# Optimization experiments

Hardware: AMD Instinct MI355X
Metric: run time of the kernel (lower is better)

## Reference

```python
import jax, jax.numpy as jnp
import numpy as np

P = 3  # patch_size; propagate_size = 3; stride = 1


def _extract_kernels(background):
    # background: [bz, nc, w, h, d] -> per-position 3x3x3 patches [bz, L, nc, 3,3,3], L = w*h*d
    bz, nc, w, h, d = background.shape
    pad = jnp.pad(background, ((0, 0), (0, 0), (1, 1), (1, 1), (1, 1)))
    shifts = [pad[:, :, i:i + w, j:j + h, k:k + d]
              for i in range(P) for j in range(P) for k in range(P)]  # 27 fixed shifts
    patches = jnp.stack(shifts, axis=-1)                      # [bz, nc, w, h, d, 27]
    patches = patches.reshape(bz, nc, w * h * d, P, P, P)     # matches torch unfold->view
    return patches.transpose(0, 2, 1, 3, 4, 5)                # [bz, L, nc, 3, 3, 3]


def _box_sum(x):
    # depthwise conv with ones[3,3,3], padding 1 (the propagation conv), done separably
    for ax in (2, 3, 4):
        n = x.shape[ax]
        cfg = [(1, 1) if a == ax else (0, 0) for a in range(x.ndim)]
        p = jnp.pad(x, cfg)
        x = (jax.lax.slice_in_dim(p, 0, n, axis=ax)
             + jax.lax.slice_in_dim(p, 1, n + 1, axis=ax)
             + jax.lax.slice_in_dim(p, 2, n + 2, axis=ax))
    return x


def _per_sample(fm, kernels, mask_i):
    # fm: [nc, w, h, d]; kernels: [L, nc, 3,3,3]; mask_i: [1, w, h, d]
    k = kernels + 1e-7
    k = k / jnp.sqrt(jnp.sum(k * k, axis=(1, 2, 3, 4), keepdims=True))
    x = fm[None]  # [1, nc, w, h, d]
    # patch-correlation: conv3d with per-sample dynamic kernels, padding=1 -> [1, L, w, h, d]
    conv_result = jax.lax.conv_general_dilated(x, k, (1, 1, 1), [(1, 1)] * 3)
    conv_result = _box_sum(conv_result)                 # propagation conv (ones kernel)
    attn = jax.nn.softmax(conv_result, axis=1)          # softmax over the L patch channels
    # conv_transpose3d(stride=1, padding=1) == conv3d with spatially flipped, IO-swapped kernel
    kt = jnp.flip(k, axis=(2, 3, 4)).transpose(1, 0, 2, 3, 4)  # [nc, L, 3, 3, 3]
    recovered = jax.lax.conv_general_dilated(attn, kt, (1, 1, 1), [(1, 1)] * 3)[0]  # [nc,w,h,d]
    recovered = recovered * mask_i / float(P ** 3)
    return recovered + fm * (1.0 - mask_i)


def setup_inputs() -> dict:
    key = jax.random.key(0)
    k1, k2 = jax.random.split(key)
    foreground = jax.random.normal(k1, (4, 64, 16, 16, 16), dtype=jnp.float32)
    mask = jnp.round(jax.random.uniform(k2, (4, 1, 16, 16, 16), dtype=jnp.float32))
    return {"foreground": foreground, "mask": mask}


def reference(foreground, mask):
    background = foreground * (1.0 - mask)   # background='same' path
    kernels = _extract_kernels(background)   # [bz, L, nc, 3, 3, 3]
    return jax.vmap(_per_sample)(foreground, kernels, mask)
```

## Files before the change

### kernel.cpp

```cpp
#include <hip/hip_runtime.h>
#include <hip/hip_bf16.h>
#include <math.h>

#define L 4096
#define NC 64
#define BZ 4
#define PS 17
#define PXD 272

typedef __attribute__((ext_vector_type(8))) short bf16x8;
typedef __attribute__((ext_vector_type(4))) float f32x4;

__device__ inline unsigned short f2bf(float f) {
    unsigned int u = __float_as_uint(f);
    return (unsigned short)((u + 0x7fffu + ((u >> 16) & 1u)) >> 16);
}
__device__ inline float bf2f(unsigned int u) { return __uint_as_float(u << 16); }
__device__ inline void unpack8(uint4 v, float* f) {
    f[0] = bf2f(v.x & 0xffffu); f[1] = bf2f(v.x >> 16);
    f[2] = bf2f(v.y & 0xffffu); f[3] = bf2f(v.y >> 16);
    f[4] = bf2f(v.z & 0xffffu); f[5] = bf2f(v.z >> 16);
    f[6] = bf2f(v.w & 0xffffu); f[7] = bf2f(v.w >> 16);
}
__device__ inline uint4 pack8(const float* f) {
    uint4 v;
    v.x = (unsigned)f2bf(f[0]) | ((unsigned)f2bf(f[1]) << 16);
    v.y = (unsigned)f2bf(f[2]) | ((unsigned)f2bf(f[3]) << 16);
    v.z = (unsigned)f2bf(f[4]) | ((unsigned)f2bf(f[5]) << 16);
    v.w = (unsigned)f2bf(f[6]) | ((unsigned)f2bf(f[7]) << 16);
    return v;
}

__device__ void box3_pad(float* A, float* B, int tid, float out[16]) {
    int x = tid >> 4, y = tid & 15;
    int base = x * PXD + y * PS;
    float t[16];
    {
        float line[16];
        #pragma unroll
        for (int z = 0; z < 16; z++) line[z] = A[base + z];
        #pragma unroll
        for (int z = 0; z < 16; z++) {
            float s = line[z];
            if (z > 0)  s += line[z - 1];
            if (z < 15) s += line[z + 1];
            t[z] = s;
        }
    }
    #pragma unroll
    for (int z = 0; z < 16; z++) B[base + z] = t[z];
    __syncthreads();
    #pragma unroll
    for (int z = 0; z < 16; z++) {
        float s = B[base + z];
        if (y > 0)  s += B[base - PS + z];
        if (y < 15) s += B[base + PS + z];
        t[z] = s;
    }
    __syncthreads();
    #pragma unroll
    for (int z = 0; z < 16; z++) A[base + z] = t[z];
    __syncthreads();
    #pragma unroll
    for (int z = 0; z < 16; z++) {
        float s = A[base + z];
        if (x > 0)  s += A[base - PXD + z];
        if (x < 15) s += A[base + PXD + z];
        out[z] = s;
    }
    __syncthreads();
}
__device__ inline void fill_pad(float* A, const float* __restrict__ g, int tid) {
    for (int i = tid; i < 4096; i += 256)
        A[(i >> 8) * PXD + ((i >> 4) & 15) * PS + (i & 15)] = g[i];
    __syncthreads();
}

__global__ void k_prep(const float* __restrict__ fm, const float* __restrict__ mask,
                       unsigned short* __restrict__ bgT, unsigned short* __restrict__ fmT,
                       unsigned short* __restrict__ bgh,
                       float* __restrict__ sfm, float* __restrict__ sbg,
                       float* __restrict__ qbg) {
    int b = blockIdx.y;
    int p = blockIdx.x * 256 + threadIdx.x;
    float m = mask[b * L + p];
    float w = 1.f - m;
    float s_f = 0.f, s_b = 0.f, q_b = 0.f;
    const float* fmb = fm + (size_t)b * NC * L + p;
    unsigned short* bghb = bgh + (size_t)b * NC * L + p;
    unsigned short tA[NC], tB[NC];
    #pragma unroll
    for (int c = 0; c < NC; c++) {
        float f = fmb[(size_t)c * L];
        float g = f * w;
        s_f += f; s_b += g; q_b += g * g;
        unsigned short gb = f2bf(g);
        tA[c] = gb;
        tB[c] = f2bf(f);
        bghb[(size_t)c * L] = gb;
    }
    unsigned short* bgTb = bgT + (size_t)b * L * NC + (size_t)p * NC;
    unsigned short* fmTb = fmT + (size_t)b * L * NC + (size_t)p * NC;
    #pragma unroll
    for (int i = 0; i < 8; i++) {
        ((uint4*)bgTb)[i] = ((const uint4*)tA)[i];
        ((uint4*)fmTb)[i] = ((const uint4*)tB)[i];
    }
    sfm[b * L + p] = s_f;
    sbg[b * L + p] = s_b;
    qbg[b * L + p] = q_b;
}

__global__ void k_stats(const float* __restrict__ sfm, const float* __restrict__ sbg,
                        const float* __restrict__ qbg,
                        float* __restrict__ invn, float* __restrict__ s2fm) {
    __shared__ float A[16 * PXD];
    __shared__ float Bf[16 * PXD];
    int b = blockIdx.x;
    int tid = threadIdx.x;
    int x = tid >> 4, y = tid & 15;
    float Q[16], Sb[16], r[16];

    fill_pad(A, qbg + b * L, tid);
    box3_pad(A, Bf, tid, Q);
    fill_pad(A, sbg + b * L, tid);
    box3_pad(A, Bf, tid, Sb);
    for (int z = 0; z < 16; z++) {
        float denom = Q[z] + 2e-7f * Sb[z] + 1.728e-11f;
        invn[b * L + x * 256 + y * 16 + z] = rsqrtf(denom);
    }
    fill_pad(A, sfm + b * L, tid);
    box3_pad(A, Bf, tid, r);
    int base = x * PXD + y * PS;
    #pragma unroll
    for (int z = 0; z < 16; z++) A[base + z] = r[z];
    __syncthreads();
    box3_pad(A, Bf, tid, r);
    for (int z = 0; z < 16; z++) s2fm[b * L + x * 256 + y * 16 + z] = r[z];
}

__global__ __launch_bounds__(256) void k_gram(const unsigned short* __restrict__ bgT,
                                              const unsigned short* __restrict__ fmT,
                                              unsigned short* __restrict__ slab,
                                              size_t slotU, int b0) {
    int zi = blockIdx.z, b = b0 + zi;
    unsigned short* Czz = slab + (size_t)zi * slotU;
    const unsigned short* bgTb = bgT + (size_t)b * L * NC;
    const unsigned short* fmTb = fmT + (size_t)b * L * NC;
    __shared__ float Gs[64][65];
    __shared__ float D1[64][65];
    int tid = threadIdx.x;
    int l0 = blockIdx.y * 64, p0 = blockIdx.x * 64;
    int w = tid >> 6, lane = tid & 63;
    int rr = lane & 15, kg = lane >> 4;

    bf16x8 a0 = *(const bf16x8*)&bgTb[(size_t)(l0 + w * 16 + rr) * NC + kg * 8];
    bf16x8 a1 = *(const bf16x8*)&bgTb[(size_t)(l0 + w * 16 + rr) * NC + 32 + kg * 8];
    f32x4 acc[4];
    #pragma unroll
    for (int pt = 0; pt < 4; pt++) {
        bf16x8 bb0 = *(const bf16x8*)&fmTb[(size_t)(p0 + pt * 16 + rr) * NC + kg * 8];
        bf16x8 bb1 = *(const bf16x8*)&fmTb[(size_t)(p0 + pt * 16 + rr) * NC + 32 + kg * 8];
        f32x4 z; z[0] = 0.f; z[1] = 0.f; z[2] = 0.f; z[3] = 0.f;
        z = __builtin_amdgcn_mfma_f32_16x16x32_bf16(a0, bb0, z, 0, 0, 0);
        z = __builtin_amdgcn_mfma_f32_16x16x32_bf16(a1, bb1, z, 0, 0, 0);
        acc[pt] = z;
    }
    #pragma unroll
    for (int pt = 0; pt < 4; pt++)
        #pragma unroll
        for (int r = 0; r < 4; r++)
            Gs[w * 16 + kg * 4 + r][pt * 16 + rr] = acc[pt][r];
    __syncthreads();
    for (int i = tid; i < 4096; i += 256) {
        int il = i >> 6, jp = i & 63;
        int lz = il & 15, pz = jp & 15;
        float v = Gs[il][jp];
        if (lz > 0 && pz > 0)   v += Gs[il - 1][jp - 1];
        if (lz < 15 && pz < 15) v += Gs[il + 1][jp + 1];
        D1[il][jp] = v;
    }
    __syncthreads();
    int row = tid >> 2, cg = (tid & 3) * 16;
    float o[16];
    #pragma unroll
    for (int k = 0; k < 16; k++) {
        int jp = cg + k;
        float v = D1[row][jp];
        if (k > 0)  v += D1[row][jp - 1];
        if (k < 15) v += D1[row][jp + 1];
        o[k] = v;
    }
    uint4* dst = (uint4*)&Czz[(size_t)(l0 + row) * L + p0 + cg];
    dst[0] = pack8(o);
    dst[1] = pack8(o + 8);
}

__global__ __launch_bounds__(256) void k_rowE(unsigned short* __restrict__ slab,
                                              size_t slotU,
                                              const float* __restrict__ s2fm,
                                              const float* __restrict__ invn, int b0) {
    __shared__ float A[16 * PXD];
    int zi = blockIdx.z, b = b0 + zi;
    const unsigned short* Czz = slab + (size_t)zi * slotU;
    unsigned short* E = slab + (size_t)zi * slotU + (size_t)L * L;
    int bx = blockIdx.x;
    int l = (bx & 7) * 512 + (bx >> 3);
    int lx = l >> 8, ly = (l >> 4) & 15;
    int tid = threadIdx.x;
    int px = tid >> 4, py = tid & 15;
    float c[16];
    #pragma unroll
    for (int z = 0; z < 16; z++) c[z] = 0.f;

    #pragma unroll
    for (int dx = -1; dx <= 1; dx++) {
        if (lx + dx < 0 || lx + dx > 15 || px + dx < 0 || px + dx > 15) continue;
        #pragma unroll
        for (int dy = -1; dy <= 1; dy++) {
            if (ly + dy < 0 || ly + dy > 15 || py + dy < 0 || py + dy > 15) continue;
            const unsigned short* src = Czz + (size_t)(l + dy * 16 + dx * 256) * L
                                        + (px + dx) * 256 + (py + dy) * 16;
            float f[16];
            unpack8(((const uint4*)src)[0], f);
            unpack8(((const uint4*)src)[1], f + 8);
            #pragma unroll
            for (int z = 0; z < 16; z++) c[z] += f[z];
        }
    }
    int base = px * PXD + py * PS;
    #pragma unroll
    for (int z = 0; z < 16; z++) A[base + z] = c[z];
    __syncthreads();
    float t[16];
    #pragma unroll
    for (int z = 0; z < 16; z++) {
        float s = A[base + z];
        if (py > 0)  s += A[base - PS + z];
        if (py < 15) s += A[base + PS + z];
        t[z] = s;
    }
    __syncthreads();
    #pragma unroll
    for (int z = 0; z < 16; z++) A[base + z] = t[z];
    __syncthreads();
    float inl = invn[(size_t)b * L + l];
    const float* s2 = s2fm + (size_t)b * L + px * 256 + py * 16;
    float o[16];
    #pragma unroll
    for (int z = 0; z < 16; z++) {
        float s = A[base + z];
        if (px > 0)  s += A[base - PXD + z];
        if (px < 15) s += A[base + PXD + z];
        o[z] = __expf((s + 1e-7f * s2[z]) * inl);
    }
    uint4* dst = (uint4*)&E[(size_t)l * L + px * 256 + py * 16];
    dst[0] = pack8(o);
    dst[1] = pack8(o + 8);
}

__global__ void k_colstat_part(unsigned short* __restrict__ slab, size_t slotU,
                               const float* __restrict__ invn, int b0) {
    int zi = blockIdx.z, b = b0 + zi;
    const unsigned short* E = slab + (size_t)zi * slotU + (size_t)L * L;
    float* ps = (float*)(slab + (size_t)zi * slotU);
    float* psi = ps + 64 * (size_t)L;
    int p8 = (blockIdx.x * 256 + threadIdx.x) * 8;
    int lc = blockIdx.y;
    const float* inv = invn + (size_t)b * L + lc * 64;
    float S[8], SI[8];
    #pragma unroll
    for (int j = 0; j < 8; j++) { S[j] = 0.f; SI[j] = 0.f; }
    const unsigned short* eb = E + (size_t)lc * 64 * L + p8;
    for (int i = 0; i < 64; i++) {
        uint4 v = *(const uint4*)(eb + (size_t)i * L);
        float f[8]; unpack8(v, f);
        float iv = inv[i];
        #pragma unroll
        for (int j = 0; j < 8; j++) { S[j] += f[j]; SI[j] += f[j] * iv; }
    }
    float4* d0 = (float4*)(ps + (size_t)lc * L + p8);
    float4* d1 = (float4*)(psi + (size_t)lc * L + p8);
    d0[0] = make_float4(S[0], S[1], S[2], S[3]);
    d0[1] = make_float4(S[4], S[5], S[6], S[7]);
    d1[0] = make_float4(SI[0], SI[1], SI[2], SI[3]);
    d1[1] = make_float4(SI[4], SI[5], SI[6], SI[7]);
}

__global__ void k_colstat_merge(unsigned short* __restrict__ slab, size_t slotU,
                                float* __restrict__ csi, float* __restrict__ Tarr, int b0) {
    int zi = blockIdx.z, b = b0 + zi;
    const float* ps = (const float*)(slab + (size_t)zi * slotU);
    const float* psi = ps + 64 * (size_t)L;
    int p = blockIdx.x * 256 + threadIdx.x;
    float s = 0.f, si = 0.f;
    for (int i = 0; i < 64; i++) { s += ps[(size_t)i * L + p]; si += psi[(size_t)i * L + p]; }
    float inv = 1.f / s;
    csi[(size_t)b * L + p] = inv;
    Tarr[(size_t)b * L + p] = si * inv;
}

__global__ void k_tbox(const float* __restrict__ Tarr, float* __restrict__ Tbox, int b0) {
    __shared__ float A[16 * PXD];
    __shared__ float Bf[16 * PXD];
    int b = b0 + blockIdx.z;
    int tid = threadIdx.x;
    fill_pad(A, Tarr + (size_t)b * L, tid);
    float res[16];
    box3_pad(A, Bf, tid, res);
    int x = tid >> 4, y = tid & 15;
    for (int z = 0; z < 16; z++) Tbox[(size_t)b * L + x * 256 + y * 16 + z] = res[z];
}

__global__ void k_sm_diagz(unsigned short* __restrict__ slab, size_t slotU,
                           const float* __restrict__ csi, const float* __restrict__ invn,
                           int b0) {
    int zi = blockIdx.z, b = b0 + zi;
    const unsigned short* E = slab + (size_t)zi * slotU + (size_t)L * L;
    unsigned short* azz = slab + (size_t)zi * slotU;
    int line = blockIdx.x * 256 + threadIdx.x;
    int l = line >> 8;
    int p0 = (line & 255) * 16;
    int lz = l & 15;
    bool hm = lz > 0, hp = lz < 15;

    float fc[16], fmv[16], fpv[16];
    const uint4* ec = (const uint4*)(E + (size_t)l * L + p0);
    unpack8(ec[0], fc); unpack8(ec[1], fc + 8);
    if (hm) {
        const uint4* em = (const uint4*)(E + (size_t)(l - 1) * L + p0);
        unpack8(em[0], fmv); unpack8(em[1], fmv + 8);
    }
    if (hp) {
        const uint4* ep = (const uint4*)(E + (size_t)(l + 1) * L + p0);
        unpack8(ep[0], fpv); unpack8(ep[1], fpv + 8);
    }
    float cs[16];
    const float4* cp = (const float4*)(csi + (size_t)b * L + p0);
    #pragma unroll
    for (int q = 0; q < 4; q++) {
        float4 v = cp[q];
        cs[q * 4] = v.x; cs[q * 4 + 1] = v.y; cs[q * 4 + 2] = v.z; cs[q * 4 + 3] = v.w;
    }
    float inl = invn[(size_t)b * L + l];
    float inlm = hm ? invn[(size_t)b * L + l - 1] : 0.f;
    float inlp = hp ? invn[(size_t)b * L + l + 1] : 0.f;
    float o[16];
    #pragma unroll
    for (int z = 0; z < 16; z++) {
        float v = fc[z] * cs[z] * inl;
        if (hm && z > 0)  v += fmv[z - 1] * cs[z - 1] * inlm;
        if (hp && z < 15) v += fpv[z + 1] * cs[z + 1] * inlp;
        o[z] = v;
    }
    uint4* dst = (uint4*)&azz[(size_t)l * L + p0];
    dst[0] = pack8(o);
    dst[1] = pack8(o + 8);
}

__global__ __launch_bounds__(256) void k_diag2t(unsigned short* __restrict__ slab,
                                                size_t slotU) {
    __shared__ float T[64][65];
    int zi = blockIdx.z;
    const unsigned short* azz = slab + (size_t)zi * slotU;
    unsigned short* Ht = slab + (size_t)zi * slotU + (size_t)L * L;
    int tid = threadIdx.x;
    int bi = blockIdx.y, bj = blockIdx.x;
    int m0 = bi * 64, p0 = bj * 64;
    int mx = bi >> 2, px = bj >> 2;
    int myb = 4 * (bi & 3), pyb = 4 * (bj & 3);
    int im = tid >> 3;
    int jp8 = (tid & 7) * 8;
    int pcol = pyb + (jp8 >> 4);

    float acc[2][8];
    #pragma unroll
    for (int g = 0; g < 2; g++)
        #pragma unroll
        for (int j = 0; j < 8; j++) acc[g][j] = 0.f;

    #pragma unroll
    for (int dx = -1; dx <= 1; dx++) {
        if (mx + dx < 0 || mx + dx > 15 || px + dx < 0 || px + dx > 15) continue;
        #pragma unroll
        for (int dy = -1; dy <= 1; dy++) {
            if (pcol + dy < 0 || pcol + dy > 15) continue;
            int D = dy * 16 + dx * 256;
            #pragma unroll
            for (int g = 0; g < 2; g++) {
                int m = im + 32 * g;
                int my = myb + (m >> 4);
                if (my + dy < 0 || my + dy > 15) continue;
                uint4 v = *(const uint4*)(azz + (size_t)(m0 + m + D) * L + p0 + jp8 + D);
                float f[8]; unpack8(v, f);
                #pragma unroll
                for (int j = 0; j < 8; j++) acc[g][j] += f[j];
            }
        }
    }
    #pragma unroll
    for (int g = 0; g < 2; g++)
        #pragma unroll
        for (int j = 0; j < 8; j++) T[im + 32 * g][jp8 + j] = acc[g][j];
    __syncthreads();
    int pr = tid >> 2, ms = (tid & 3) * 16;
    float o[16];
    #pragma unroll
    for (int i = 0; i < 16; i++) o[i] = T[ms + i][pr];
    uint4* dst = (uint4*)&Ht[(size_t)(p0 + pr) * L + m0 + ms];
    dst[0] = pack8(o);
    dst[1] = pack8(o + 8);
}

__global__ __launch_bounds__(256) void k_mm(unsigned short* __restrict__ slab, size_t slotU,
                                            const unsigned short* __restrict__ bgh, int b0) {
    int zi = blockIdx.z, b = b0 + zi;
    const unsigned short* Ht = slab + (size_t)zi * slotU + (size_t)L * L;
    float* part = (float*)(slab + (size_t)zi * slotU);
    const unsigned short* bghb = bgh + (size_t)b * NC * L;
    int tid = threadIdx.x;
    int w = tid >> 6, lane = tid & 63;
    int rr = lane & 15, kg = lane >> 4;
    int p0 = blockIdx.x * 64;
    int k0 = blockIdx.y * 512;

    f32x4 acc[4];
    #pragma unroll
    for (int pt = 0; pt < 4; pt++) { acc[pt][0] = 0.f; acc[pt][1] = 0.f; acc[pt][2] = 0.f; acc[pt][3] = 0.f; }

    for (int kk = 0; kk < 16; kk++) {
        int kb = k0 + kk * 32 + kg * 8;
        bf16x8 a = *(const bf16x8*)&bghb[(size_t)(w * 16 + rr) * L + kb];
        #pragma unroll
        for (int pt = 0; pt < 4; pt++) {
            bf16x8 bb = *(const bf16x8*)&Ht[(size_t)(p0 + pt * 16 + rr) * L + kb];
            acc[pt] = __builtin_amdgcn_mfma_f32_16x16x32_bf16(a, bb, acc[pt], 0, 0, 0);
        }
    }
    float* pp = part + (size_t)blockIdx.y * NC * L;
    #pragma unroll
    for (int pt = 0; pt < 4; pt++)
        #pragma unroll
        for (int r = 0; r < 4; r++)
            pp[(size_t)(w * 16 + kg * 4 + r) * L + p0 + pt * 16 + rr] = acc[pt][r];
}

__global__ void k_epilogue(unsigned short* __restrict__ slab, size_t slotU,
                           const float* __restrict__ Tbox, const float* __restrict__ mask,
                           const float* __restrict__ fm, float* __restrict__ out, int b0) {
    int zi = blockIdx.z, b = b0 + zi;
    const float* part = (const float*)(slab + (size_t)zi * slotU);
    int idx4 = (blockIdx.x * 256 + threadIdx.x) * 4;
    int p = idx4 & 4095;
    float4 s = make_float4(0.f, 0.f, 0.f, 0.f);
    #pragma unroll
    for (int i = 0; i < 8; i++) {
        float4 v = *(const float4*)(part + (size_t)i * NC * L + idx4);
        s.x += v.x; s.y += v.y; s.z += v.z; s.w += v.w;
    }
    float4 tb = *(const float4*)(Tbox + (size_t)b * L + p);
    float4 mk = *(const float4*)(mask + (size_t)b * L + p);
    float4 fv = *(const float4*)(fm + (size_t)b * NC * L + idx4);
    float4 o;
    o.x = (s.x + 1e-7f * tb.x) * mk.x * (1.f / 27.f) + fv.x * (1.f - mk.x);
    o.y = (s.y + 1e-7f * tb.y) * mk.y * (1.f / 27.f) + fv.y * (1.f - mk.y);
    o.z = (s.z + 1e-7f * tb.z) * mk.z * (1.f / 27.f) + fv.z * (1.f - mk.z);
    o.w = (s.w + 1e-7f * tb.w) * mk.w * (1.f / 27.f) + fv.w * (1.f - mk.w);
    *(float4*)(out + (size_t)b * NC * L + idx4) = o;
}

extern "C" void kernel_launch(void* const* d_in, const int* in_sizes, int n_in,
                              void* d_out, int out_size, void* d_ws, size_t ws_size,
                              hipStream_t stream) {
    const float* fm = (const float*)d_in[0];
    const float* mask = (const float*)d_in[1];
    float* out = (float*)d_out;

    unsigned short* bgT = (unsigned short*)d_ws;
    unsigned short* fmT = bgT + (size_t)BZ * L * NC;
    unsigned short* bgh = fmT + (size_t)BZ * L * NC;
    float* sfm  = (float*)(bgh + (size_t)BZ * L * NC);
    float* sbg  = sfm + (size_t)BZ * L;
    float* qbg  = sbg + (size_t)BZ * L;
    float* invn = qbg + (size_t)BZ * L;
    float* s2fm = invn + (size_t)BZ * L;
    float* csi  = s2fm + (size_t)BZ * L;
    float* Tarr = csi + (size_t)BZ * L;
    float* Tbox = Tarr + (size_t)BZ * L;
    unsigned short* slab = (unsigned short*)(Tbox + (size_t)BZ * L);

    const size_t slotU = 2 * (size_t)L * L;
    size_t fixedBytes = (char*)slab - (char*)d_ws;
    size_t avail = ws_size > fixedBytes ? ws_size - fixedBytes : 0;
    int ns = (int)(avail / (slotU * sizeof(unsigned short)));
    if (ns >= 4) ns = 4; else if (ns >= 2) ns = 2; else ns = 1;

    k_prep<<<dim3(16, BZ), 256, 0, stream>>>(fm, mask, bgT, fmT, bgh, sfm, sbg, qbg);
    k_stats<<<BZ, 256, 0, stream>>>(sfm, sbg, qbg, invn, s2fm);

    for (int b0 = 0; b0 < BZ; b0 += ns) {
        int nb = (BZ - b0) < ns ? (BZ - b0) : ns;
        k_gram<<<dim3(64, 64, nb), 256, 0, stream>>>(bgT, fmT, slab, slotU, b0);
        k_rowE<<<dim3(4096, 1, nb), 256, 0, stream>>>(slab, slotU, s2fm, invn, b0);
        k_colstat_part<<<dim3(2, 64, nb), 256, 0, stream>>>(slab, slotU, invn, b0);
        k_colstat_merge<<<dim3(16, 1, nb), 256, 0, stream>>>(slab, slotU, csi, Tarr, b0);
        k_tbox<<<dim3(1, 1, nb), 256, 0, stream>>>(Tarr, Tbox, b0);
        k_sm_diagz<<<dim3(4096, 1, nb), 256, 0, stream>>>(slab, slotU, csi, invn, b0);
        k_diag2t<<<dim3(64, 64, nb), 256, 0, stream>>>(slab, slotU);
        k_mm<<<dim3(64, 8, nb), 256, 0, stream>>>(slab, slotU, bgh, b0);
        k_epilogue<<<dim3(256, 1, nb), 256, 0, stream>>>(slab, slotU, Tbox, mask, fm, out, b0);
    }
}
```

Baseline: 653.4 us.

## Batch stencil loads into predicated registers and drop shared-memory passes

Several kernels change at once. In k_rowE and k_diag2t, the nine stencil loads are now issued up front with clamped addresses and 0/1 weights, so they can all be in flight together instead of each sitting behind a branch. k_rowE also does its y-direction box sum with warp shuffles rather than a shared-memory round trip, and k_gram fuses two stencil passes into one so the D1 buffer and a barrier go away. The colstat loop is unrolled by four, the diag1 neighbour loads become unconditional, k_mm's inner loop is unrolled by two, and launch bounds are raised, at the cost of more registers and some redundant loads and arithmetic.

```diff
diff --git a/kernel.cpp b/kernel.cpp
--- a/kernel.cpp
+++ b/kernel.cpp
@@ -148,7 +148,6 @@
     const unsigned short* bgTb = bgT + (size_t)b * L * NC;
     const unsigned short* fmTb = fmT + (size_t)b * L * NC;
     __shared__ float Gs[64][65];
-    __shared__ float D1[64][65];
     int tid = threadIdx.x;
     int l0 = blockIdx.y * 64, p0 = blockIdx.x * 64;
     int w = tid >> 6, lane = tid & 63;
@@ -172,23 +171,27 @@
         for (int r = 0; r < 4; r++)
             Gs[w * 16 + kg * 4 + r][pt * 16 + rr] = acc[pt][r];
     __syncthreads();
-    for (int i = tid; i < 4096; i += 256) {
-        int il = i >> 6, jp = i & 63;
-        int lz = il & 15, pz = jp & 15;
-        float v = Gs[il][jp];
-        if (lz > 0 && pz > 0)   v += Gs[il - 1][jp - 1];
-        if (lz < 15 && pz < 15) v += Gs[il + 1][jp + 1];
-        D1[il][jp] = v;
-    }
-    __syncthreads();
+
     int row = tid >> 2, cg = (tid & 3) * 16;
+    int lz = row & 15;
+    float wl0 = lz > 0 ? 1.f : 0.f, wl2 = lz < 15 ? 1.f : 0.f;
+    int rm = row > 0 ? row - 1 : 0, rp = row < 63 ? row + 1 : 63;
     float o[16];
     #pragma unroll
     for (int k = 0; k < 16; k++) {
-        int jp = cg + k;
-        float v = D1[row][jp];
-        if (k > 0)  v += D1[row][jp - 1];
-        if (k < 15) v += D1[row][jp + 1];
+        float v = 0.f;
+        #pragma unroll
+        for (int e = -1; e <= 1; e++) {
+            if (k + e < 0 || k + e > 15) continue;
+            #pragma unroll
+            for (int d = -1; d <= 1; d++) {
+                if (k + e + d < 0 || k + e + d > 15) continue;
+                int col = cg + k + e + d;
+                if (d == 0)       v += Gs[row][col];
+                else if (d == -1) v += wl0 * Gs[rm][col];
+                else              v += wl2 * Gs[rp][col];
+            }
+        }
         o[k] = v;
     }
     uint4* dst = (uint4*)&Czz[(size_t)(l0 + row) * L + p0 + cg];
@@ -196,10 +199,10 @@
     dst[1] = pack8(o + 8);
 }
 
-__global__ __launch_bounds__(256) void k_rowE(unsigned short* __restrict__ slab,
-                                              size_t slotU,
-                                              const float* __restrict__ s2fm,
-                                              const float* __restrict__ invn, int b0) {
+__global__ __launch_bounds__(256, 4) void k_rowE(unsigned short* __restrict__ slab,
+                                                 size_t slotU,
+                                                 const float* __restrict__ s2fm,
+                                                 const float* __restrict__ invn, int b0) {
     __shared__ float A[16 * PXD];
     int zi = blockIdx.z, b = b0 + zi;
     const unsigned short* Czz = slab + (size_t)zi * slotU;
@@ -209,40 +212,47 @@
     int lx = l >> 8, ly = (l >> 4) & 15;
     int tid = threadIdx.x;
     int px = tid >> 4, py = tid & 15;
+    size_t own = (size_t)l * L + px * 256 + py * 16;
+
+    uint4 v0[9], v1[9];
+    float wgt[9];
+    #pragma unroll
+    for (int t = 0; t < 9; t++) {
+        int dx = t / 3 - 1, dy = t % 3 - 1;
+        bool ok = (unsigned)(lx + dx) < 16u && (unsigned)(px + dx) < 16u &&
+                  (unsigned)(ly + dy) < 16u && (unsigned)(py + dy) < 16u;
+        size_t off = ok ? ((size_t)(l + dy * 16 + dx * 256) * L
+                           + (px + dx) * 256 + (py + dy) * 16)
+                        : own;
+        const uint4* s4 = (const uint4*)(Czz + off);
+        v0[t] = s4[0];
+        v1[t] = s4[1];
+        wgt[t] = ok ? 1.f : 0.f;
+    }
     float c[16];
     #pragma unroll
     for (int z = 0; z < 16; z++) c[z] = 0.f;
-
-    #pragma unroll
-    for (int dx = -1; dx <= 1; dx++) {
-        if (lx + dx < 0 || lx + dx > 15 || px + dx < 0 || px + dx > 15) continue;
-        #pragma unroll
-        for (int dy = -1; dy <= 1; dy++) {
-            if (ly + dy < 0 || ly + dy > 15 || py + dy < 0 || py + dy > 15) continue;
-            const unsigned short* src = Czz + (size_t)(l + dy * 16 + dx * 256) * L
-                                        + (px + dx) * 256 + (py + dy) * 16;
-            float f[16];
-            unpack8(((const uint4*)src)[0], f);
-            unpack8(((const uint4*)src)[1], f + 8);
-            #pragma unroll
-            for (int z = 0; z < 16; z++) c[z] += f[z];
-        }
+    #pragma unroll
+    for (int t = 0; t < 9; t++) {
+        float f[16];
+        unpack8(v0[t], f);
+        unpack8(v1[t], f + 8);
+        #pragma unroll
+        for (int z = 0; z < 16; z++) c[z] += wgt[t] * f[z];
+    }
+    float t16[16];
+    #pragma unroll
+    for (int z = 0; z < 16; z++) {
+        float up = __shfl_up(c[z], 1);
+        float dn = __shfl_down(c[z], 1);
+        float s = c[z];
+        if (py > 0)  s += up;
+        if (py < 15) s += dn;
+        t16[z] = s;
     }
     int base = px * PXD + py * PS;
     #pragma unroll
-    for (int z = 0; z < 16; z++) A[base + z] = c[z];
-    __syncthreads();
-    float t[16];
-    #pragma unroll
-    for (int z = 0; z < 16; z++) {
-        float s = A[base + z];
-        if (py > 0)  s += A[base - PS + z];
-        if (py < 15) s += A[base + PS + z];
-        t[z] = s;
-    }
-    __syncthreads();
-    #pragma unroll
-    for (int z = 0; z < 16; z++) A[base + z] = t[z];
+    for (int z = 0; z < 16; z++) A[base + z] = t16[z];
     __syncthreads();
     float inl = invn[(size_t)b * L + l];
     const float* s2 = s2fm + (size_t)b * L + px * 256 + py * 16;
@@ -254,7 +264,7 @@
         if (px < 15) s += A[base + PXD + z];
         o[z] = __expf((s + 1e-7f * s2[z]) * inl);
     }
-    uint4* dst = (uint4*)&E[(size_t)l * L + px * 256 + py * 16];
+    uint4* dst = (uint4*)&E[own];
     dst[0] = pack8(o);
     dst[1] = pack8(o + 8);
 }
@@ -272,10 +282,23 @@
     #pragma unroll
     for (int j = 0; j < 8; j++) { S[j] = 0.f; SI[j] = 0.f; }
     const unsigned short* eb = E + (size_t)lc * 64 * L + p8;
-    for (int i = 0; i < 64; i++) {
-        uint4 v = *(const uint4*)(eb + (size_t)i * L);
-        float f[8]; unpack8(v, f);
-        float iv = inv[i];
+    for (int i = 0; i < 64; i += 4) {
+        uint4 va = *(const uint4*)(eb + (size_t)(i + 0) * L);
+        uint4 vb = *(const uint4*)(eb + (size_t)(i + 1) * L);
+        uint4 vc = *(const uint4*)(eb + (size_t)(i + 2) * L);
+        uint4 vd = *(const uint4*)(eb + (size_t)(i + 3) * L);
+        float f[8];
+        float iv;
+        unpack8(va, f); iv = inv[i];
+        #pragma unroll
+        for (int j = 0; j < 8; j++) { S[j] += f[j]; SI[j] += f[j] * iv; }
+        unpack8(vb, f); iv = inv[i + 1];
+        #pragma unroll
+        for (int j = 0; j < 8; j++) { S[j] += f[j]; SI[j] += f[j] * iv; }
+        unpack8(vc, f); iv = inv[i + 2];
+        #pragma unroll
+        for (int j = 0; j < 8; j++) { S[j] += f[j]; SI[j] += f[j] * iv; }
+        unpack8(vd, f); iv = inv[i + 3];
         #pragma unroll
         for (int j = 0; j < 8; j++) { S[j] += f[j]; SI[j] += f[j] * iv; }
     }
@@ -322,19 +345,21 @@
     int l = line >> 8;
     int p0 = (line & 255) * 16;
     int lz = l & 15;
-    bool hm = lz > 0, hp = lz < 15;
+    float wm = lz > 0 ? 1.f : 0.f, wp = lz < 15 ? 1.f : 0.f;
+    int lm = lz > 0 ? l - 1 : l, lp = lz < 15 ? l + 1 : l;
+
+    const uint4* ec = (const uint4*)(E + (size_t)l * L + p0);
+    const uint4* em = (const uint4*)(E + (size_t)lm * L + p0);
+    const uint4* ep = (const uint4*)(E + (size_t)lp * L + p0);
+    uint4 c0 = ec[0], c1 = ec[1];
+    uint4 m0v = em[0], m1v = em[1];
+    uint4 p0v = ep[0], p1v = ep[1];
 
     float fc[16], fmv[16], fpv[16];
-    const uint4* ec = (const uint4*)(E + (size_t)l * L + p0);
-    unpack8(ec[0], fc); unpack8(ec[1], fc + 8);
-    if (hm) {
-        const uint4* em = (const uint4*)(E + (size_t)(l - 1) * L + p0);
-        unpack8(em[0], fmv); unpack8(em[1], fmv + 8);
-    }
-    if (hp) {
-        const uint4* ep = (const uint4*)(E + (size_t)(l + 1) * L + p0);
-        unpack8(ep[0], fpv); unpack8(ep[1], fpv + 8);
-    }
+    unpack8(c0, fc); unpack8(c1, fc + 8);
+    unpack8(m0v, fmv); unpack8(m1v, fmv + 8);
+    unpack8(p0v, fpv); unpack8(p1v, fpv + 8);
+
     float cs[16];
     const float4* cp = (const float4*)(csi + (size_t)b * L + p0);
     #pragma unroll
@@ -343,14 +368,14 @@
         cs[q * 4] = v.x; cs[q * 4 + 1] = v.y; cs[q * 4 + 2] = v.z; cs[q * 4 + 3] = v.w;
     }
     float inl = invn[(size_t)b * L + l];
-    float inlm = hm ? invn[(size_t)b * L + l - 1] : 0.f;
-    float inlp = hp ? invn[(size_t)b * L + l + 1] : 0.f;
+    float inlm = invn[(size_t)b * L + lm] * wm;
+    float inlp = invn[(size_t)b * L + lp] * wp;
     float o[16];
     #pragma unroll
     for (int z = 0; z < 16; z++) {
         float v = fc[z] * cs[z] * inl;
-        if (hm && z > 0)  v += fmv[z - 1] * cs[z - 1] * inlm;
-        if (hp && z < 15) v += fpv[z + 1] * cs[z + 1] * inlp;
+        if (z > 0)  v += fmv[z - 1] * cs[z - 1] * inlm;
+        if (z < 15) v += fpv[z + 1] * cs[z + 1] * inlp;
         o[z] = v;
     }
     uint4* dst = (uint4*)&azz[(size_t)l * L + p0];
@@ -358,8 +383,8 @@
     dst[1] = pack8(o + 8);
 }
 
-__global__ __launch_bounds__(256) void k_diag2t(unsigned short* __restrict__ slab,
-                                                size_t slotU) {
+__global__ __launch_bounds__(256, 4) void k_diag2t(unsigned short* __restrict__ slab,
+                                                   size_t slotU) {
     __shared__ float T[64][65];
     int zi = blockIdx.z;
     const unsigned short* azz = slab + (size_t)zi * slotU;
@@ -373,29 +398,37 @@
     int jp8 = (tid & 7) * 8;
     int pcol = pyb + (jp8 >> 4);
 
+    uint4 vv[2][9];
+    float ww[2][9];
+    #pragma unroll
+    for (int t = 0; t < 9; t++) {
+        int dx = t / 3 - 1, dy = t % 3 - 1;
+        int D = dy * 16 + dx * 256;
+        bool okc = (unsigned)(mx + dx) < 16u && (unsigned)(px + dx) < 16u &&
+                   (unsigned)(pcol + dy) < 16u;
+        #pragma unroll
+        for (int g = 0; g < 2; g++) {
+            int m = im + 32 * g;
+            int my = myb + (m >> 4);
+            bool ok = okc && (unsigned)(my + dy) < 16u;
+            size_t off = ok ? ((size_t)(m0 + m + D) * L + p0 + jp8 + D)
+                            : ((size_t)(m0 + m) * L + p0 + jp8);
+            vv[g][t] = *(const uint4*)(azz + off);
+            ww[g][t] = ok ? 1.f : 0.f;
+        }
+    }
     float acc[2][8];
     #pragma unroll
     for (int g = 0; g < 2; g++)
         #pragma unroll
         for (int j = 0; j < 8; j++) acc[g][j] = 0.f;
-
-    #pragma unroll
-    for (int dx = -1; dx <= 1; dx++) {
-        if (mx + dx < 0 || mx + dx > 15 || px + dx < 0 || px + dx > 15) continue;
-        #pragma unroll
-        for (int dy = -1; dy <= 1; dy++) {
-            if (pcol + dy < 0 || pcol + dy > 15) continue;
-            int D = dy * 16 + dx * 256;
+    #pragma unroll
+    for (int t = 0; t < 9; t++) {
+        #pragma unroll
+        for (int g = 0; g < 2; g++) {
+            float f[8]; unpack8(vv[g][t], f);
             #pragma unroll
-            for (int g = 0; g < 2; g++) {
-                int m = im + 32 * g;
-                int my = myb + (m >> 4);
-                if (my + dy < 0 || my + dy > 15) continue;
-                uint4 v = *(const uint4*)(azz + (size_t)(m0 + m + D) * L + p0 + jp8 + D);
-                float f[8]; unpack8(v, f);
-                #pragma unroll
-                for (int j = 0; j < 8; j++) acc[g][j] += f[j];
-            }
+            for (int j = 0; j < 8; j++) acc[g][j] += ww[g][t] * f[j];
         }
     }
     #pragma unroll
@@ -428,6 +461,7 @@
     #pragma unroll
     for (int pt = 0; pt < 4; pt++) { acc[pt][0] = 0.f; acc[pt][1] = 0.f; acc[pt][2] = 0.f; acc[pt][3] = 0.f; }
 
+    #pragma unroll 2
     for (int kk = 0; kk < 16; kk++) {
         int kb = k0 + kk * 32 + kg * 8;
         bf16x8 a = *(const bf16x8*)&bghb[(size_t)(w * 16 + rr) * L + kb];
```

Result: slower. 1.092 ms (+67.2%).
